# Optimization experiments

Hardware: AMD Instinct MI355X
Metric: run time of the kernel (lower is better)

Reference implementation:

```python
import jax, jax.numpy as jnp
import numpy as np

N_USERS, N_ITEMS, D = 16384, 8192, 64
IMG_D, TXT_D = 4096, 384
TOPK = 10
LAMBDA = 0.9         # args.lambda_coeff
NNZ = 786432
N_TOTAL = N_USERS + N_ITEMS


def l2norm(x, eps=1e-12):
    # F.normalize(p=2, dim=1)
    return x / jnp.maximum(jnp.linalg.norm(x, axis=-1, keepdims=True), eps)


def build_knn_graph(feats):
    """build_sim + build_knn_normalized_graph (sparse, sym norm).
    Returns row-sparse KNN graph as (values [N,k], indices [N,k])."""
    z = l2norm(feats)
    sim = z @ z.T                          # [N, N] cosine similarity
    vals, inds = jax.lax.top_k(sim, TOPK)  # [N, k]
    rowsum = vals.sum(axis=1)              # degree
    d_inv_sqrt = jnp.where(rowsum > 0, rowsum, 1.0) ** -0.5
    vals = vals * d_inv_sqrt[:, None] * d_inv_sqrt[inds]  # D^-1/2 A D^-1/2
    return vals, inds


def knn_mm(vals, inds, x):
    # sparse.mm with row-sparse [N,k] graph: out[i] = sum_k vals[i,k]*x[inds[i,k]]
    return jnp.einsum('nk,nkd->nd', vals, x[inds])


def setup_inputs() -> dict:
    key = jax.random.key(0)
    ks = jax.random.split(key, 16)
    xav = lambda k, shp: jax.random.normal(k, shp, jnp.float32) * (2.0 / (shp[0] + shp[-1])) ** 0.5
    return dict(
        adj_rows=jax.random.randint(ks[0], (NNZ,), 0, N_TOTAL, jnp.int32),
        adj_cols=jax.random.randint(ks[1], (NNZ,), 0, N_TOTAL, jnp.int32),
        adj_vals=jax.random.uniform(ks[2], (NNZ,), jnp.float32) / 32.0,
        image_feats=jax.random.normal(ks[3], (N_ITEMS, IMG_D), jnp.float32),
        text_feats=jax.random.normal(ks[4], (N_ITEMS, TXT_D), jnp.float32),
        user_emb=xav(ks[5], (N_USERS, D)),
        item_emb=xav(ks[6], (N_ITEMS, D)),
        img_w=xav(ks[7], (IMG_D, D)), img_b=jnp.zeros((D,), jnp.float32),
        txt_w=xav(ks[8], (TXT_D, D)), txt_b=jnp.zeros((D,), jnp.float32),
        q_w1=xav(ks[9], (D, D)), q_b1=jnp.zeros((D,), jnp.float32),
        q_w2=xav(ks[10], (D, 1)),
        gc_w=xav(ks[11], (2, D, D)), gc_b=jnp.zeros((2, D), jnp.float32),
        bi_w=xav(ks[12], (2, D, D)), bi_b=jnp.zeros((2, D), jnp.float32),
    )


def reference(adj_rows, adj_cols, adj_vals, image_feats, text_feats,
              user_emb, item_emb, img_w, img_b, txt_w, txt_b,
              q_w1, q_b1, q_w2, gc_w, gc_b, bi_w, bi_b):
    # original (init-time) modal graphs from raw features
    io_v, io_i = build_knn_graph(image_feats)
    to_v, to_i = build_knn_graph(text_feats)
    # projected modal features + dynamic graphs (build_item_graph=True)
    img_f = image_feats @ img_w + img_b
    txt_f = text_feats @ txt_w + txt_b
    in_v, in_i = build_knn_graph(img_f)
    tn_v, tn_i = build_knn_graph(txt_f)
    # one propagation layer over (1-l)*new_adj + l*orig_adj (separable for layers=1)
    e = item_emb
    img_e = (1 - LAMBDA) * knn_mm(in_v, in_i, e) + LAMBDA * knn_mm(io_v, io_i, e)
    txt_e = (1 - LAMBDA) * knn_mm(tn_v, tn_i, e) + LAMBDA * knn_mm(to_v, to_i, e)
    # attention-weighted fusion
    query = lambda x: jnp.tanh(x @ q_w1 + q_b1) @ q_w2   # [N_ITEMS, 1]
    att = jnp.concatenate([query(img_e), query(txt_e)], axis=-1)
    w = jax.nn.softmax(att, axis=-1)
    h = w[:, :1] * img_e + w[:, 1:] * txt_e
    # NGCF user-item propagation (dropout p=0 -> identity)
    ego = jnp.concatenate([user_emb, item_emb], axis=0)   # [N_TOTAL, D]
    all_e = [ego]
    for i in range(2):
        side = jax.ops.segment_sum(adj_vals[:, None] * ego[adj_cols], adj_rows,
                                   num_segments=N_TOTAL)
        s = jax.nn.leaky_relu(side @ gc_w[i] + gc_b[i])
        b = jax.nn.leaky_relu((ego * side) @ bi_w[i] + bi_b[i])
        ego = s + b
        all_e.append(l2norm(ego))
    all_e = jnp.mean(jnp.stack(all_e, axis=1), axis=1)
    u_g, i_g = all_e[:N_USERS], all_e[N_USERS:]
    i_g = i_g + l2norm(h)
    return u_g, i_g, img_e, txt_e, h
```

## Files before the change

### kernel.cpp

```cpp
#include <hip/hip_runtime.h>
#include <hip/hip_bf16.h>
#include <math.h>

#define N_USERS 16384
#define N_ITEMS 8192
#define N_TOTAL 24576
#define EMB_D 64
#define IMG_DIM 4096
#define TXT_DIM 384
#define K_TOP 10
#define N_CAND 16
#define NNZ_E 786432
#define NTILE 64
#define TRI_BLOCKS (NTILE * (NTILE + 1) / 2)
#define MIR_BLOCKS (NTILE * (NTILE - 1) / 2)
#define LDS_ST 129

typedef _Float16 f16x8 __attribute__((ext_vector_type(8)));
typedef float f32x4 __attribute__((ext_vector_type(4)));

#define AS1 __attribute__((address_space(1)))
#define AS3 __attribute__((address_space(3)))

__device__ __forceinline__ float leaky01(float x){ return x >= 0.f ? x : 0.01f * x; }

__device__ __forceinline__ void gld16(const void* g, void* l) {
  __builtin_amdgcn_global_load_lds((const AS1 unsigned int*)g, (AS3 unsigned int*)l, 16, 0, 0);
}

__device__ __forceinline__ bool beats(float v, int i, float u, int j) {
  return v > u || (v == u && i < j);
}

__device__ __forceinline__ float h2f(unsigned short u) {
  _Float16 h = __builtin_bit_cast(_Float16, u);
  return (float)h;
}
__device__ __forceinline__ unsigned short f2h(float v) {
  _Float16 h = (_Float16)v;
  return __builtin_bit_cast(unsigned short, h);
}

__global__ __launch_bounds__(256) void fill_map_k(int* __restrict__ map) {
  int b = blockIdx.x * 256 + threadIdx.x;
  if (b >= TRI_BLOCKS) return;
  int tileX, tileY;
  if (b < 1792) {
    int s = b >> 6, w = b & 63;
    int sy = 0, rem = 7;
    while (s >= rem) { s -= rem; sy++; rem--; }
    int sx = sy + 1 + s;
    tileY = sy * 8 + (w >> 3);
    tileX = sx * 8 + (w & 7);
  } else {
    int b2 = b - 1792;
    int sd = b2 / 36, w = b2 - sd * 36;
    int i = 0, rem = 8;
    while (w >= rem) { w -= rem; i++; rem--; }
    tileY = sd * 8 + i;
    tileX = sd * 8 + i + w;
  }
  map[b] = (tileY << 16) | tileX;
}

template<int TRI>
__global__ __launch_bounds__(256) void sim_mfma_k(const unsigned short* __restrict__ Zh,
                                                  unsigned short* __restrict__ C, int K, int r0,
                                                  const int* __restrict__ tile_map) {
  __shared__ unsigned short smA[128 * 32];
  __shared__ unsigned short smB[128 * 32];
  const int tid = threadIdx.x;
  const int lane = tid & 63;
  const int wid = tid >> 6;
  const int wr = wid >> 1, wc = wid & 1;

  int tileX, tileY;
  if (TRI) {
    int tm = tile_map[blockIdx.x];
    tileY = tm >> 16;
    tileX = tm & 0xffff;
  } else {
    tileX = blockIdx.x; tileY = blockIdx.y;
  }

  const int bRow = r0 + tileY * 128;
  const int bCol = tileX * 128;

  f32x4 acc[4][4];
  const f32x4 fzero = {0.f, 0.f, 0.f, 0.f};
  #pragma unroll
  for (int m = 0; m < 4; m++)
    #pragma unroll
    for (int n = 0; n < 4; n++) acc[m][n] = fzero;

  const int u0 = (wid * 2 + 0) * 64 + lane;
  const int u1 = (wid * 2 + 1) * 64 + lane;
  const int ar0 = u0 >> 2, ac0 = (u0 & 3) * 8;
  const int ar1 = u1 >> 2, ac1 = (u1 & 3) * 8;
  const unsigned offA0 = ((unsigned)(bRow + ar0) * (unsigned)K + (unsigned)ac0) * 2u;
  const unsigned offA1 = ((unsigned)(bRow + ar1) * (unsigned)K + (unsigned)ac1) * 2u;
  const unsigned offB0 = ((unsigned)(bCol + ar0) * (unsigned)K + (unsigned)ac0) * 2u;
  const unsigned offB1 = ((unsigned)(bCol + ar1) * (unsigned)K + (unsigned)ac1) * 2u;
  const char* Zb = (const char*)Zh;
  unsigned short* ldsA0 = smA + (wid * 2 + 0) * 512;
  unsigned short* ldsA1 = smA + (wid * 2 + 1) * 512;
  unsigned short* ldsB0 = smB + (wid * 2 + 0) * 512;
  unsigned short* ldsB1 = smB + (wid * 2 + 1) * 512;

  const int kc = lane >> 4;
  const int fr = lane & 15;

  for (unsigned kb = 0; kb < (unsigned)K * 2u; kb += 64u) {
    __syncthreads();
    gld16(Zb + (offA0 + kb), ldsA0);
    gld16(Zb + (offA1 + kb), ldsA1);
    gld16(Zb + (offB0 + kb), ldsB0);
    gld16(Zb + (offB1 + kb), ldsB1);
    __syncthreads();

    f16x8 a[4], b[4];
    #pragma unroll
    for (int m = 0; m < 4; m++)
      a[m] = *(const f16x8*)&smA[(wr * 64 + m * 16 + fr) * 32 + kc * 8];
    #pragma unroll
    for (int n = 0; n < 4; n++)
      b[n] = *(const f16x8*)&smB[(wc * 64 + n * 16 + fr) * 32 + kc * 8];
    #pragma unroll
    for (int m = 0; m < 4; m++)
      #pragma unroll
      for (int n = 0; n < 4; n++)
        acc[m][n] = __builtin_amdgcn_mfma_f32_16x16x32_f16(a[m], b[n], acc[m][n], 0, 0, 0);
  }

  const int crow = tileY * 128 + wr * 64 + (lane >> 4) * 4;
  const int ccol = bCol + wc * 64 + (lane & 15);
  #pragma unroll
  for (int m = 0; m < 4; m++)
    #pragma unroll
    for (int n = 0; n < 4; n++)
      #pragma unroll
      for (int r = 0; r < 4; r++)
        C[(size_t)(crow + m * 16 + r) * N_ITEMS + ccol + n * 16] = f2h(acc[m][n][r]);
}

__global__ __launch_bounds__(256) void tri_mirror_k(unsigned short* __restrict__ C) {
  __shared__ unsigned short t[128 * LDS_ST];
  int b = blockIdx.x;
  int ty = 0, rem = NTILE - 1;
  while (b >= rem) { b -= rem; ty++; rem--; }
  int tx = ty + 1 + b;
  const int tid = threadIdx.x;

  #pragma unroll
  for (int it = 0; it < 8; it++) {
    int idx = it * 2048 + tid * 8;
    int r = idx >> 7, c = idx & 127;
    uint4 v = *(const uint4*)&C[(size_t)(ty * 128 + r) * N_ITEMS + tx * 128 + c];
    const unsigned short* pv = (const unsigned short*)&v;
    #pragma unroll
    for (int j = 0; j < 8; j++) t[r * LDS_ST + c + j] = pv[j];
  }
  __syncthreads();

  #pragma unroll
  for (int it = 0; it < 8; it++) {
    int idx = it * 2048 + tid * 8;
    int orow = idx >> 7;
    int ocol = idx & 127;
    unsigned short buf[8];
    #pragma unroll
    for (int j = 0; j < 8; j++) buf[j] = t[(ocol + j) * LDS_ST + orow];
    *(uint4*)&C[(size_t)(tx * 128 + orow) * N_ITEMS + ty * 128 + ocol] = *(const uint4*)buf;
  }
}

__device__ __forceinline__ void ins4(float val, int idx, float tv[4], int ti[4]) {
  if (beats(val, idx, tv[3], ti[3])) {
    tv[3] = val; ti[3] = idx;
    if (beats(tv[3], ti[3], tv[2], ti[2])) { float a=tv[2];int b=ti[2]; tv[2]=tv[3];ti[2]=ti[3]; tv[3]=a;ti[3]=b; }
    if (beats(tv[2], ti[2], tv[1], ti[1])) { float a=tv[1];int b=ti[1]; tv[1]=tv[2];ti[1]=ti[2]; tv[2]=a;ti[2]=b; }
    if (beats(tv[1], ti[1], tv[0], ti[0])) { float a=tv[0];int b=ti[0]; tv[0]=tv[1];ti[0]=ti[1]; tv[1]=a;ti[1]=b; }
  }
}

__global__ __launch_bounds__(256) void topk16h_k(const unsigned short* __restrict__ sim,
                                                 int r0, int* __restrict__ cand) {
  int row = blockIdx.x * 4 + (threadIdx.x >> 6);
  int lane = threadIdx.x & 63;
  const uint4* s8 = reinterpret_cast<const uint4*>(sim + (size_t)row * N_ITEMS);

  float tv[4]; int ti[4];
  #pragma unroll
  for (int k = 0; k < 4; k++) { tv[k] = -INFINITY; ti[k] = 0x7fffffff; }
  unsigned long long ext0 = 0ull, ext1 = 0ull;

  for (int i = 0; i < 16; i++) {
    uint4 v = s8[i * 64 + lane];
    int base = (i * 64 + lane) * 8;
    ins4(h2f(v.x & 0xffff), base + 0, tv, ti);
    ins4(h2f(v.x >> 16),    base + 1, tv, ti);
    ins4(h2f(v.y & 0xffff), base + 2, tv, ti);
    ins4(h2f(v.y >> 16),    base + 3, tv, ti);
    ins4(h2f(v.z & 0xffff), base + 4, tv, ti);
    ins4(h2f(v.z >> 16),    base + 5, tv, ti);
    ins4(h2f(v.w & 0xffff), base + 6, tv, ti);
    ins4(h2f(v.w >> 16),    base + 7, tv, ti);
  }
  int nvalid = 4;
  for (int t = 0; t < N_CAND; t++) {
    float bv = tv[0]; int bi = ti[0];
    for (int o = 32; o; o >>= 1) {
      float ov = __shfl_xor(bv, o, 64);
      int   oi = __shfl_xor(bi, o, 64);
      if (beats(ov, oi, bv, bi)) { bv = ov; bi = oi; }
    }
    if (tv[0] == bv && ti[0] == bi) {
      int slot = ((bi >> 9) << 3) | (bi & 7);
      if (slot < 64) ext0 |= 1ull << slot; else ext1 |= 1ull << (slot - 64);
      tv[0]=tv[1];ti[0]=ti[1]; tv[1]=tv[2];ti[1]=ti[2]; tv[2]=tv[3];ti[2]=ti[3];
      tv[3]=-INFINITY; ti[3]=0x7fffffff;
      nvalid--;
      if (nvalid == 0) {
        for (int i = 0; i < 16; i++) {
          uint4 v = s8[i * 64 + lane];
          int base = (i * 64 + lane) * 8;
          float vv[8] = {h2f(v.x & 0xffff), h2f(v.x >> 16), h2f(v.y & 0xffff), h2f(v.y >> 16),
                         h2f(v.z & 0xffff), h2f(v.z >> 16), h2f(v.w & 0xffff), h2f(v.w >> 16)};
          #pragma unroll
          for (int q = 0; q < 8; q++) {
            int slot2 = i * 8 + q;
            bool used = (slot2 < 64) ? ((ext0 >> slot2) & 1ull) : ((ext1 >> (slot2 - 64)) & 1ull);
            if (!used) ins4(vv[q], base + q, tv, ti);
          }
        }
        nvalid = 4;
      }
    }
    if (lane == 0) cand[(size_t)(r0 + row) * N_CAND + t] = bi;
  }
}

__global__ __launch_bounds__(256) void refine_k(const float* __restrict__ X, int K,
                                                const float* __restrict__ invn,
                                                const int* __restrict__ cand,
                                                float* __restrict__ vals, int* __restrict__ inds,
                                                float* __restrict__ dis) {
  __shared__ __align__(16) float xr[4096];
  __shared__ float dots[N_CAND];
  int row = blockIdx.x;
  int tid = threadIdx.x, lane = tid & 63, wid = tid >> 6;
  for (int j = tid; j < K; j += 256) xr[j] = X[(size_t)row * K + j];
  __syncthreads();
  for (int c = wid; c < N_CAND; c += 4) {
    int ci = cand[(size_t)row * N_CAND + c];
    const float* xc = X + (size_t)ci * K;
    float p = 0.f;
    if (K == 4096) {
      const float4* xc4 = reinterpret_cast<const float4*>(xc);
      const float4* xr4 = reinterpret_cast<const float4*>(xr);
      for (int it = 0; it < 16; it++) {
        float4 a = xr4[it * 64 + lane];
        float4 g = xc4[it * 64 + lane];
        p += a.x * g.x + a.y * g.y + a.z * g.z + a.w * g.w;
      }
    } else {
      for (int j = lane; j < K; j += 64) p += xr[j] * xc[j];
    }
    for (int o = 32; o; o >>= 1) p += __shfl_xor(p, o, 64);
    if (lane == 0) dots[c] = p;
  }
  __syncthreads();
  if (tid == 0) {
    float v[N_CAND]; int id[N_CAND];
    float ir = invn[row];
    for (int c = 0; c < N_CAND; c++) {
      id[c] = cand[(size_t)row * N_CAND + c];
      v[c] = dots[c] * ir * invn[id[c]];
    }
    for (int a = 1; a < N_CAND; a++) {
      float av = v[a]; int ai = id[a];
      int b = a - 1;
      while (b >= 0 && beats(av, ai, v[b], id[b])) { v[b+1]=v[b]; id[b+1]=id[b]; b--; }
      v[b+1] = av; id[b+1] = ai;
    }
    float sum = 0.f;
    for (int t = 0; t < K_TOP; t++) {
      vals[(size_t)row * K_TOP + t] = v[t];
      inds[(size_t)row * K_TOP + t] = id[t];
      sum += v[t];
    }
    float rs = sum > 0.f ? sum : 1.0f;
    dis[row] = 1.0f / sqrtf(rs);
  }
}

__global__ __launch_bounds__(256) void scale_vals_k(float* __restrict__ vals,
                                                    const int* __restrict__ inds,
                                                    const float* __restrict__ dis, int tot) {
  int idx = blockIdx.x * 256 + threadIdx.x;
  if (idx < tot) {
    int i = idx / K_TOP;
    vals[idx] *= dis[i] * dis[inds[idx]];
  }
}

__global__ __launch_bounds__(256) void norm_cast_fused_k(const float* __restrict__ x,
                                                         float* __restrict__ invn,
                                                         unsigned short* __restrict__ zh, int K) {
  __shared__ __align__(16) float xr[4096];
  __shared__ float red[256];
  int r = blockIdx.x;
  const float* xp = x + (size_t)r * K;
  float ss = 0.f;
  for (int j = threadIdx.x; j < K; j += 256) { float v = xp[j]; xr[j] = v; ss += v * v; }
  red[threadIdx.x] = ss; __syncthreads();
  for (int s = 128; s > 0; s >>= 1) {
    if (threadIdx.x < s) red[threadIdx.x] += red[threadIdx.x + s];
    __syncthreads();
  }
  float inv = 1.f / fmaxf(sqrtf(red[0]), 1e-12f);
  if (threadIdx.x == 0) invn[r] = inv;
  for (int j = threadIdx.x; j < K; j += 256) {
    zh[(size_t)r * K + j] = f2h(xr[j] * inv);
  }
}

__global__ __launch_bounds__(256) void linear_splitk_k(const float* __restrict__ X,
                                                       const float* __restrict__ W,
                                                       const float* __restrict__ b,
                                                       float* __restrict__ outp, int K, int KS) {
  __shared__ float As[64][17];
  __shared__ float Ws[16][64];
  int br = blockIdx.x, ks = blockIdx.y;
  int tid = threadIdx.x, tr = tid >> 4, tc = tid & 15;
  int k0 = ks * KS, k1 = k0 + KS;
  int lrow = tid >> 2, lk = (tid & 3) * 4;
  int wrow = tid >> 4, wcol = (tid & 15) * 4;
  float acc[4][4] = {};
  for (int kb = k0; kb < k1; kb += 16) {
    __syncthreads();
    float4 xv = *(const float4*)&X[(size_t)(br * 64 + lrow) * K + kb + lk];
    As[lrow][lk + 0] = xv.x; As[lrow][lk + 1] = xv.y;
    As[lrow][lk + 2] = xv.z; As[lrow][lk + 3] = xv.w;
    *(float4*)&Ws[wrow][wcol] = *(const float4*)&W[(size_t)(kb + wrow) * 64 + wcol];
    __syncthreads();
    #pragma unroll
    for (int k = 0; k < 16; k++) {
      float a[4], w[4];
      #pragma unroll
      for (int i = 0; i < 4; i++) a[i] = As[tr * 4 + i][k];
      #pragma unroll
      for (int j = 0; j < 4; j++) w[j] = Ws[k][tc * 4 + j];
      #pragma unroll
      for (int i = 0; i < 4; i++)
        #pragma unroll
        for (int j = 0; j < 4; j++) acc[i][j] += a[i] * w[j];
    }
  }
  #pragma unroll
  for (int i = 0; i < 4; i++)
    #pragma unroll
    for (int j = 0; j < 4; j++) {
      float v = acc[i][j];
      if (ks == 0) v += b[tc * 4 + j];
      atomicAdd(&outp[(size_t)(br * 64 + tr * 4 + i) * 64 + tc * 4 + j], v);
    }
}

__global__ __launch_bounds__(256) void fuse_knn_k(const float* __restrict__ av, const int* __restrict__ ai,
                                                  const float* __restrict__ bv, const int* __restrict__ bi_,
                                                  const float* __restrict__ e, float* __restrict__ outp,
                                                  float lam) {
  int i = blockIdx.x * 4 + (threadIdx.x >> 6), d = threadIdx.x & 63;
  float sa = 0.f, sb = 0.f;
  #pragma unroll
  for (int k = 0; k < K_TOP; k++) {
    sa += av[(size_t)i * K_TOP + k] * e[(size_t)ai[(size_t)i * K_TOP + k] * 64 + d];
    sb += bv[(size_t)i * K_TOP + k] * e[(size_t)bi_[(size_t)i * K_TOP + k] * 64 + d];
  }
  outp[(size_t)i * 64 + d] = (1.f - lam) * sa + lam * sb;
}

__global__ __launch_bounds__(64) void attn_k(const float* __restrict__ img_e, const float* __restrict__ txt_e,
                                             const float* __restrict__ qw1, const float* __restrict__ qb1,
                                             const float* __restrict__ qw2, float* __restrict__ h) {
  __shared__ float W1[64][64];
  __shared__ float sI[64], sT[64];
  int t = threadIdx.x; int i = blockIdx.x;
  for (int k = 0; k < 64; k++) W1[k][t] = qw1[k * 64 + t];
  sI[t] = img_e[(size_t)i * 64 + t];
  sT[t] = txt_e[(size_t)i * 64 + t];
  __syncthreads();
  float yi = qb1[t], yt = qb1[t];
  #pragma unroll 16
  for (int k = 0; k < 64; k++) { yi += sI[k] * W1[k][t]; yt += sT[k] * W1[k][t]; }
  float w2 = qw2[t];
  float pi = tanhf(yi) * w2, pt = tanhf(yt) * w2;
  for (int o = 32; o > 0; o >>= 1) { pi += __shfl_xor(pi, o, 64); pt += __shfl_xor(pt, o, 64); }
  float m = fmaxf(pi, pt);
  float ei = expf(pi - m), et = expf(pt - m);
  float den = ei + et;
  float w0 = ei / den, w1v = et / den;
  h[(size_t)i * 64 + t] = w0 * sI[t] + w1v * sT[t];
}

__global__ __launch_bounds__(256) void hist_k(const int* __restrict__ rows, int* __restrict__ cnt) {
  int e = blockIdx.x * 256 + threadIdx.x;
  if (e < NNZ_E) atomicAdd(&cnt[rows[e]], 1);
}

__global__ __launch_bounds__(256) void scan_k(const int* __restrict__ cnt,
                                              int* __restrict__ starts,
                                              int* __restrict__ cursor) {
  __shared__ int part[256];
  int t = threadIdx.x;
  int base = t * (N_TOTAL / 256);
  int s = 0;
  for (int j = 0; j < N_TOTAL / 256; j++) s += cnt[base + j];
  part[t] = s;
  __syncthreads();
  for (int off = 1; off < 256; off <<= 1) {
    int v = part[t];
    int u = (t >= off) ? part[t - off] : 0;
    __syncthreads();
    part[t] = v + u;
    __syncthreads();
  }
  int run = (t > 0) ? part[t - 1] : 0;
  for (int j = 0; j < N_TOTAL / 256; j++) {
    starts[base + j] = run;
    cursor[base + j] = run;
    run += cnt[base + j];
  }
  if (t == 255) starts[N_TOTAL] = run;
}

__global__ __launch_bounds__(256) void place_k(const int* __restrict__ rows,
                                               const int* __restrict__ cols,
                                               const float* __restrict__ vals,
                                               int* __restrict__ cursor,
                                               int* __restrict__ cols_s,
                                               float* __restrict__ vals_s) {
  int e = blockIdx.x * 256 + threadIdx.x;
  if (e < NNZ_E) {
    int p = atomicAdd(&cursor[rows[e]], 1);
    cols_s[p] = cols[e];
    vals_s[p] = vals[e];
  }
}

__global__ __launch_bounds__(256) void gather_gcn_k(const int* __restrict__ starts,
                                                    const int* __restrict__ cols_s,
                                                    const float* __restrict__ vals_s,
                                                    const float* __restrict__ ego,
                                                    float* __restrict__ side) {
  int row = blockIdx.x * 4 + (threadIdx.x >> 6);
  int d = threadIdx.x & 63;
  int s = starts[row], e = starts[row + 1];
  float acc = 0.f;
  for (int i = s; i < e; i++) {
    acc += vals_s[i] * ego[(size_t)cols_s[i] * 64 + d];
  }
  side[(size_t)row * 64 + d] = acc;
}

__global__ __launch_bounds__(256) void gcn_k(const float* __restrict__ side, const float* __restrict__ ego,
                                             const float* __restrict__ gw, const float* __restrict__ gb,
                                             const float* __restrict__ bw, const float* __restrict__ bb,
                                             float* __restrict__ outp) {
  __shared__ float W1[64][64], W2[64][64];
  __shared__ float S[4][64], E[4][64];
  int t = threadIdx.x & 63, rb = threadIdx.x >> 6;
  int r = blockIdx.x * 4 + rb;
  for (int idx = threadIdx.x; idx < 4096; idx += 256) {
    W1[idx >> 6][idx & 63] = gw[idx];
    W2[idx >> 6][idx & 63] = bw[idx];
  }
  S[rb][t] = side[(size_t)r * 64 + t];
  E[rb][t] = ego[(size_t)r * 64 + t];
  __syncthreads();
  float s = gb[t], b = bb[t];
  #pragma unroll 16
  for (int k = 0; k < 64; k++) {
    float sv = S[rb][k];
    s += sv * W1[k][t];
    b += E[rb][k] * sv * W2[k][t];
  }
  outp[(size_t)r * 64 + t] = leaky01(s) + leaky01(b);
}

__global__ __launch_bounds__(256) void l2acc_k(const float* __restrict__ ego, float* __restrict__ acc) {
  int r = blockIdx.x * 4 + (threadIdx.x >> 6), d = threadIdx.x & 63;
  float v = ego[(size_t)r * 64 + d];
  float ss = v * v;
  for (int o = 32; o > 0; o >>= 1) ss += __shfl_xor(ss, o, 64);
  float inv = 1.f / fmaxf(sqrtf(ss), 1e-12f);
  acc[(size_t)r * 64 + d] += v * inv;
}

__global__ __launch_bounds__(256) void init_ego_k(const float* __restrict__ ue, const float* __restrict__ ie,
                                                  float* __restrict__ ego, float* __restrict__ acc) {
  int r = blockIdx.x * 4 + (threadIdx.x >> 6), d = threadIdx.x & 63;
  float v = (r < N_USERS) ? ue[(size_t)r * 64 + d] : ie[(size_t)(r - N_USERS) * 64 + d];
  ego[(size_t)r * 64 + d] = v;
  acc[(size_t)r * 64 + d] = v;
}

__global__ __launch_bounds__(256) void final_k(const float* __restrict__ acc, const float* __restrict__ h,
                                               float* __restrict__ u_g, float* __restrict__ i_g) {
  int r = blockIdx.x * 4 + (threadIdx.x >> 6), d = threadIdx.x & 63;
  float m = acc[(size_t)r * 64 + d] * (1.0f / 3.0f);
  if (r < N_USERS) {
    u_g[(size_t)r * 64 + d] = m;
  } else {
    int i = r - N_USERS;
    float hv = h[(size_t)i * 64 + d];
    float ss = hv * hv;
    for (int o = 32; o > 0; o >>= 1) ss += __shfl_xor(ss, o, 64);
    float inv = 1.f / fmaxf(sqrtf(ss), 1e-12f);
    i_g[(size_t)i * 64 + d] = m + hv * inv;
  }
}

static void build_graph(hipStream_t stream, const float* feats, int K, float* invn,
                        unsigned short* zh, unsigned short* sim, int stripe, int* cand,
                        const int* tile_map, float* vals, int* inds, float* dis) {
  norm_cast_fused_k<<<N_ITEMS, 256, 0, stream>>>(feats, invn, zh, K);
  if (stripe >= N_ITEMS) {
    sim_mfma_k<1><<<TRI_BLOCKS, 256, 0, stream>>>(zh, sim, K, 0, tile_map);
    tri_mirror_k<<<MIR_BLOCKS, 256, 0, stream>>>(sim);
    topk16h_k<<<N_ITEMS / 4, 256, 0, stream>>>(sim, 0, cand);
  } else {
    for (int r0 = 0; r0 < N_ITEMS; r0 += stripe) {
      int rows = (N_ITEMS - r0) < stripe ? (N_ITEMS - r0) : stripe;
      dim3 g(N_ITEMS / 128, rows / 128);
      sim_mfma_k<0><<<g, 256, 0, stream>>>(zh, sim, K, r0, tile_map);
      topk16h_k<<<rows / 4, 256, 0, stream>>>(sim, r0, cand);
    }
  }
  refine_k<<<N_ITEMS, 256, 0, stream>>>(feats, K, invn, cand, vals, inds, dis);
  int tot = N_ITEMS * K_TOP;
  scale_vals_k<<<(tot + 255) / 256, 256, 0, stream>>>(vals, inds, dis, tot);
}

extern "C" void kernel_launch(void* const* d_in, const int* in_sizes, int n_in,
                              void* d_out, int out_size, void* d_ws, size_t ws_size,
                              hipStream_t stream) {
  const int*   adj_rows   = (const int*)d_in[0];
  const int*   adj_cols   = (const int*)d_in[1];
  const float* adj_vals   = (const float*)d_in[2];
  const float* image_feats= (const float*)d_in[3];
  const float* text_feats = (const float*)d_in[4];
  const float* user_emb   = (const float*)d_in[5];
  const float* item_emb   = (const float*)d_in[6];
  const float* img_w      = (const float*)d_in[7];
  const float* img_b      = (const float*)d_in[8];
  const float* txt_w      = (const float*)d_in[9];
  const float* txt_b      = (const float*)d_in[10];
  const float* q_w1       = (const float*)d_in[11];
  const float* q_b1       = (const float*)d_in[12];
  const float* q_w2       = (const float*)d_in[13];
  const float* gc_w       = (const float*)d_in[14];
  const float* gc_b       = (const float*)d_in[15];
  const float* bi_w       = (const float*)d_in[16];
  const float* bi_b       = (const float*)d_in[17];

  float* out  = (float*)d_out;
  float* u_g  = out;
  float* i_g  = u_g + (size_t)N_USERS * 64;
  float* imgE = i_g + (size_t)N_ITEMS * 64;
  float* txtE = imgE + (size_t)N_ITEMS * 64;
  float* hOut = txtE + (size_t)N_ITEMS * 64;

  float* W = (float*)d_ws;
  size_t off = 0;
  auto alloc = [&](size_t n) { float* q = W + off; off += n; return q; };
  float* inv_io = alloc(N_ITEMS);
  float* inv_to = alloc(N_ITEMS);
  float* inv_in = alloc(N_ITEMS);
  float* inv_tn = alloc(N_ITEMS);
  float* img_f  = alloc((size_t)N_ITEMS * 64);
  float* txt_f  = alloc((size_t)N_ITEMS * 64);
  float* vals0 = alloc(N_ITEMS * K_TOP); int* inds0 = (int*)alloc(N_ITEMS * K_TOP);
  float* vals1 = alloc(N_ITEMS * K_TOP); int* inds1 = (int*)alloc(N_ITEMS * K_TOP);
  float* vals2 = alloc(N_ITEMS * K_TOP); int* inds2 = (int*)alloc(N_ITEMS * K_TOP);
  float* vals3 = alloc(N_ITEMS * K_TOP); int* inds3 = (int*)alloc(N_ITEMS * K_TOP);
  float* dis0 = alloc(N_ITEMS);
  float* dis1 = alloc(N_ITEMS);
  float* dis2 = alloc(N_ITEMS);
  float* dis3 = alloc(N_ITEMS);
  int*   cand = (int*)alloc((size_t)N_ITEMS * N_CAND);
  int*   tile_map = (int*)alloc(TRI_BLOCKS);
  float* ego_a = alloc((size_t)N_TOTAL * 64);
  float* ego_b = alloc((size_t)N_TOTAL * 64);
  float* side  = alloc((size_t)N_TOTAL * 64);
  float* acc   = alloc((size_t)N_TOTAL * 64);
  int* csr_cnt    = (int*)alloc(N_TOTAL);
  int* csr_starts = (int*)alloc(N_TOTAL + 1);
  int* csr_cursor = (int*)alloc(N_TOTAL);
  int* csr_cols   = (int*)alloc(NNZ_E);
  float* csr_vals = alloc(NNZ_E);
  unsigned short* zh = (unsigned short*)alloc(((size_t)N_ITEMS * IMG_DIM) / 2);
  unsigned short* sim = (unsigned short*)(W + off);

  size_t used_bytes = off * 4;
  size_t avail_b = (ws_size > used_bytes) ? (ws_size - used_bytes) : 0;
  long stripe_l = (long)((avail_b / ((size_t)N_ITEMS * 2)) / 128) * 128;
  if (stripe_l > N_ITEMS) stripe_l = N_ITEMS;
  if (stripe_l < 128) stripe_l = 128;
  int stripe = (int)stripe_l;

  fill_map_k<<<(TRI_BLOCKS + 255) / 256, 256, 0, stream>>>(tile_map);

  hipMemsetAsync(csr_cnt, 0, N_TOTAL * sizeof(int), stream);
  hist_k<<<(NNZ_E + 255) / 256, 256, 0, stream>>>(adj_rows, csr_cnt);
  scan_k<<<1, 256, 0, stream>>>(csr_cnt, csr_starts, csr_cursor);
  place_k<<<(NNZ_E + 255) / 256, 256, 0, stream>>>(adj_rows, adj_cols, adj_vals,
                                                   csr_cursor, csr_cols, csr_vals);

  build_graph(stream, image_feats, IMG_DIM, inv_io, zh, sim, stripe, cand, tile_map, vals0, inds0, dis0);
  build_graph(stream, text_feats,  TXT_DIM, inv_to, zh, sim, stripe, cand, tile_map, vals1, inds1, dis1);

  hipMemsetAsync(img_f, 0, (size_t)N_ITEMS * 64 * sizeof(float), stream);
  hipMemsetAsync(txt_f, 0, (size_t)N_ITEMS * 64 * sizeof(float), stream);
  linear_splitk_k<<<dim3(N_ITEMS / 64, 4), 256, 0, stream>>>(image_feats, img_w, img_b, img_f, IMG_DIM, IMG_DIM / 4);
  linear_splitk_k<<<dim3(N_ITEMS / 64, 4), 256, 0, stream>>>(text_feats,  txt_w, txt_b, txt_f, TXT_DIM, TXT_DIM / 4);

  build_graph(stream, img_f, 64, inv_in, zh, sim, stripe, cand, tile_map, vals2, inds2, dis2);
  build_graph(stream, txt_f, 64, inv_tn, zh, sim, stripe, cand, tile_map, vals3, inds3, dis3);

  const float lam = 0.9f;
  fuse_knn_k<<<N_ITEMS / 4, 256, 0, stream>>>(vals2, inds2, vals0, inds0, item_emb, imgE, lam);
  fuse_knn_k<<<N_ITEMS / 4, 256, 0, stream>>>(vals3, inds3, vals1, inds1, item_emb, txtE, lam);

  attn_k<<<N_ITEMS, 64, 0, stream>>>(imgE, txtE, q_w1, q_b1, q_w2, hOut);

  init_ego_k<<<N_TOTAL / 4, 256, 0, stream>>>(user_emb, item_emb, ego_a, acc);

  gather_gcn_k<<<N_TOTAL / 4, 256, 0, stream>>>(csr_starts, csr_cols, csr_vals, ego_a, side);
  gcn_k<<<N_TOTAL / 4, 256, 0, stream>>>(side, ego_a, gc_w, gc_b, bi_w, bi_b, ego_b);
  l2acc_k<<<N_TOTAL / 4, 256, 0, stream>>>(ego_b, acc);

  gather_gcn_k<<<N_TOTAL / 4, 256, 0, stream>>>(csr_starts, csr_cols, csr_vals, ego_b, side);
  gcn_k<<<N_TOTAL / 4, 256, 0, stream>>>(side, ego_b, gc_w + 4096, gc_b + 64, bi_w + 4096, bi_b + 64, ego_a);
  l2acc_k<<<N_TOTAL / 4, 256, 0, stream>>>(ego_a, acc);

  final_k<<<N_TOTAL / 4, 256, 0, stream>>>(acc, hOut, u_g, i_g);
}
```

Measured before the change: 2.406 ms.

## Store triangular sim tiles as fp32, then convert and mirror in one pass

The triangular MFMA kernel now writes fp32 tiles to a separate fp32 buffer. A new conv_mirror kernel, covering all triangle tiles, converts them to fp16, writes the upper tile and the transposed mirror tile. The fp16 conversion thus moves out of the GEMM epilogue into the mirror pass. This doubles the bytes the GEMM writes and adds an extra full fp32 read, and it needs the workspace to hold both a half and a float similarity matrix, falling back to the striped path otherwise.

```diff
diff --git a/kernel.cpp b/kernel.cpp
--- a/kernel.cpp
+++ b/kernel.cpp
@@ -13,7 +13,6 @@
 #define NNZ_E 786432
 #define NTILE 64
 #define TRI_BLOCKS (NTILE * (NTILE + 1) / 2)
-#define MIR_BLOCKS (NTILE * (NTILE - 1) / 2)
 #define LDS_ST 129
 
 typedef _Float16 f16x8 __attribute__((ext_vector_type(8)));
@@ -63,10 +62,9 @@
   map[b] = (tileY << 16) | tileX;
 }
 
-template<int TRI>
-__global__ __launch_bounds__(256) void sim_mfma_k(const unsigned short* __restrict__ Zh,
-                                                  unsigned short* __restrict__ C, int K, int r0,
-                                                  const int* __restrict__ tile_map) {
+__global__ __launch_bounds__(256) void sim_mfma_tri_k(const unsigned short* __restrict__ Zh,
+                                                      float* __restrict__ C, int K,
+                                                      const int* __restrict__ tile_map) {
   __shared__ unsigned short smA[128 * 32];
   __shared__ unsigned short smB[128 * 32];
   const int tid = threadIdx.x;
@@ -74,16 +72,10 @@
   const int wid = tid >> 6;
   const int wr = wid >> 1, wc = wid & 1;
 
-  int tileX, tileY;
-  if (TRI) {
-    int tm = tile_map[blockIdx.x];
-    tileY = tm >> 16;
-    tileX = tm & 0xffff;
-  } else {
-    tileX = blockIdx.x; tileY = blockIdx.y;
-  }
-
-  const int bRow = r0 + tileY * 128;
+  int tm = tile_map[blockIdx.x];
+  const int tileY = tm >> 16;
+  const int tileX = tm & 0xffff;
+  const int bRow = tileY * 128;
   const int bCol = tileX * 128;
 
   f32x4 acc[4][4];
@@ -132,6 +124,75 @@
         acc[m][n] = __builtin_amdgcn_mfma_f32_16x16x32_f16(a[m], b[n], acc[m][n], 0, 0, 0);
   }
 
+  const int crow = bRow + wr * 64 + (lane >> 4) * 4;
+  const int ccol = bCol + wc * 64 + (lane & 15);
+  #pragma unroll
+  for (int m = 0; m < 4; m++)
+    #pragma unroll
+    for (int n = 0; n < 4; n++)
+      #pragma unroll
+      for (int r = 0; r < 4; r++)
+        C[(size_t)(crow + m * 16 + r) * N_ITEMS + ccol + n * 16] = acc[m][n][r];
+}
+
+__global__ __launch_bounds__(256) void sim_mfma_rect_k(const unsigned short* __restrict__ Zh,
+                                                       unsigned short* __restrict__ C, int K, int r0) {
+  __shared__ unsigned short smA[128 * 32];
+  __shared__ unsigned short smB[128 * 32];
+  const int tid = threadIdx.x;
+  const int lane = tid & 63;
+  const int wid = tid >> 6;
+  const int wr = wid >> 1, wc = wid & 1;
+  const int tileX = blockIdx.x, tileY = blockIdx.y;
+
+  const int bRow = r0 + tileY * 128;
+  const int bCol = tileX * 128;
+
+  f32x4 acc[4][4];
+  const f32x4 fzero = {0.f, 0.f, 0.f, 0.f};
+  #pragma unroll
+  for (int m = 0; m < 4; m++)
+    #pragma unroll
+    for (int n = 0; n < 4; n++) acc[m][n] = fzero;
+
+  const int u0 = (wid * 2 + 0) * 64 + lane;
+  const int u1 = (wid * 2 + 1) * 64 + lane;
+  const int ar0 = u0 >> 2, ac0 = (u0 & 3) * 8;
+  const int ar1 = u1 >> 2, ac1 = (u1 & 3) * 8;
+  const size_t rowA0 = (size_t)(bRow + ar0) * K;
+  const size_t rowA1 = (size_t)(bRow + ar1) * K;
+  const size_t rowB0 = (size_t)(bCol + ar0) * K;
+  const size_t rowB1 = (size_t)(bCol + ar1) * K;
+  unsigned short* ldsA0 = smA + (wid * 2 + 0) * 512;
+  unsigned short* ldsA1 = smA + (wid * 2 + 1) * 512;
+  unsigned short* ldsB0 = smB + (wid * 2 + 0) * 512;
+  unsigned short* ldsB1 = smB + (wid * 2 + 1) * 512;
+
+  const int kc = lane >> 4;
+  const int fr = lane & 15;
+
+  for (int k0 = 0; k0 < K; k0 += 32) {
+    __syncthreads();
+    gld16(Zh + rowA0 + k0 + ac0, ldsA0);
+    gld16(Zh + rowA1 + k0 + ac1, ldsA1);
+    gld16(Zh + rowB0 + k0 + ac0, ldsB0);
+    gld16(Zh + rowB1 + k0 + ac1, ldsB1);
+    __syncthreads();
+
+    f16x8 a[4], b[4];
+    #pragma unroll
+    for (int m = 0; m < 4; m++)
+      a[m] = *(const f16x8*)&smA[(wr * 64 + m * 16 + fr) * 32 + kc * 8];
+    #pragma unroll
+    for (int n = 0; n < 4; n++)
+      b[n] = *(const f16x8*)&smB[(wc * 64 + n * 16 + fr) * 32 + kc * 8];
+    #pragma unroll
+    for (int m = 0; m < 4; m++)
+      #pragma unroll
+      for (int n = 0; n < 4; n++)
+        acc[m][n] = __builtin_amdgcn_mfma_f32_16x16x32_f16(a[m], b[n], acc[m][n], 0, 0, 0);
+  }
+
   const int crow = tileY * 128 + wr * 64 + (lane >> 4) * 4;
   const int ccol = bCol + wc * 64 + (lane & 15);
   #pragma unroll
@@ -143,23 +204,30 @@
         C[(size_t)(crow + m * 16 + r) * N_ITEMS + ccol + n * 16] = f2h(acc[m][n][r]);
 }
 
-__global__ __launch_bounds__(256) void tri_mirror_k(unsigned short* __restrict__ C) {
+__global__ __launch_bounds__(256) void conv_mirror_k(const float* __restrict__ Cf,
+                                                     unsigned short* __restrict__ Ch,
+                                                     const int* __restrict__ tile_map) {
   __shared__ unsigned short t[128 * LDS_ST];
-  int b = blockIdx.x;
-  int ty = 0, rem = NTILE - 1;
-  while (b >= rem) { b -= rem; ty++; rem--; }
-  int tx = ty + 1 + b;
+  int tm = tile_map[blockIdx.x];
+  const int ty = tm >> 16;
+  const int tx = tm & 0xffff;
   const int tid = threadIdx.x;
 
   #pragma unroll
   for (int it = 0; it < 8; it++) {
     int idx = it * 2048 + tid * 8;
     int r = idx >> 7, c = idx & 127;
-    uint4 v = *(const uint4*)&C[(size_t)(ty * 128 + r) * N_ITEMS + tx * 128 + c];
-    const unsigned short* pv = (const unsigned short*)&v;
-    #pragma unroll
-    for (int j = 0; j < 8; j++) t[r * LDS_ST + c + j] = pv[j];
-  }
+    const float* src = &Cf[(size_t)(ty * 128 + r) * N_ITEMS + tx * 128 + c];
+    float4 v0 = *(const float4*)(src);
+    float4 v1 = *(const float4*)(src + 4);
+    unsigned short buf[8];
+    buf[0] = f2h(v0.x); buf[1] = f2h(v0.y); buf[2] = f2h(v0.z); buf[3] = f2h(v0.w);
+    buf[4] = f2h(v1.x); buf[5] = f2h(v1.y); buf[6] = f2h(v1.z); buf[7] = f2h(v1.w);
+    *(uint4*)&Ch[(size_t)(ty * 128 + r) * N_ITEMS + tx * 128 + c] = *(const uint4*)buf;
+    #pragma unroll
+    for (int j = 0; j < 8; j++) t[r * LDS_ST + c + j] = buf[j];
+  }
+  if (tx == ty) return;
   __syncthreads();
 
   #pragma unroll
@@ -170,7 +238,7 @@
     unsigned short buf[8];
     #pragma unroll
     for (int j = 0; j < 8; j++) buf[j] = t[(ocol + j) * LDS_ST + orow];
-    *(uint4*)&C[(size_t)(tx * 128 + orow) * N_ITEMS + ty * 128 + ocol] = *(const uint4*)buf;
+    *(uint4*)&Ch[(size_t)(tx * 128 + orow) * N_ITEMS + ty * 128 + ocol] = *(const uint4*)buf;
   }
 }
 
@@ -523,19 +591,20 @@
 }
 
 static void build_graph(hipStream_t stream, const float* feats, int K, float* invn,
-                        unsigned short* zh, unsigned short* sim, int stripe, int* cand,
-                        const int* tile_map, float* vals, int* inds, float* dis) {
+                        unsigned short* zh, unsigned short* simh, float* simf,
+                        int tri_ok, int stripe, int* cand, const int* tile_map,
+                        float* vals, int* inds, float* dis) {
   norm_cast_fused_k<<<N_ITEMS, 256, 0, stream>>>(feats, invn, zh, K);
-  if (stripe >= N_ITEMS) {
-    sim_mfma_k<1><<<TRI_BLOCKS, 256, 0, stream>>>(zh, sim, K, 0, tile_map);
-    tri_mirror_k<<<MIR_BLOCKS, 256, 0, stream>>>(sim);
-    topk16h_k<<<N_ITEMS / 4, 256, 0, stream>>>(sim, 0, cand);
+  if (tri_ok) {
+    sim_mfma_tri_k<<<TRI_BLOCKS, 256, 0, stream>>>(zh, simf, K, tile_map);
+    conv_mirror_k<<<TRI_BLOCKS, 256, 0, stream>>>(simf, simh, tile_map);
+    topk16h_k<<<N_ITEMS / 4, 256, 0, stream>>>(simh, 0, cand);
   } else {
     for (int r0 = 0; r0 < N_ITEMS; r0 += stripe) {
       int rows = (N_ITEMS - r0) < stripe ? (N_ITEMS - r0) : stripe;
       dim3 g(N_ITEMS / 128, rows / 128);
-      sim_mfma_k<0><<<g, 256, 0, stream>>>(zh, sim, K, r0, tile_map);
-      topk16h_k<<<rows / 4, 256, 0, stream>>>(sim, r0, cand);
+      sim_mfma_rect_k<<<g, 256, 0, stream>>>(zh, simh, K, r0);
+      topk16h_k<<<rows / 4, 256, 0, stream>>>(simh, r0, cand);
     }
   }
   refine_k<<<N_ITEMS, 256, 0, stream>>>(feats, K, invn, cand, vals, inds, dis);
@@ -601,14 +670,22 @@
   int* csr_cols   = (int*)alloc(NNZ_E);
   float* csr_vals = alloc(NNZ_E);
   unsigned short* zh = (unsigned short*)alloc(((size_t)N_ITEMS * IMG_DIM) / 2);
-  unsigned short* sim = (unsigned short*)(W + off);
-
+
+  const size_t simh_b = (size_t)N_ITEMS * N_ITEMS * 2;
+  const size_t simf_b = (size_t)N_ITEMS * N_ITEMS * 4;
   size_t used_bytes = off * 4;
   size_t avail_b = (ws_size > used_bytes) ? (ws_size - used_bytes) : 0;
-  long stripe_l = (long)((avail_b / ((size_t)N_ITEMS * 2)) / 128) * 128;
-  if (stripe_l > N_ITEMS) stripe_l = N_ITEMS;
-  if (stripe_l < 128) stripe_l = 128;
-  int stripe = (int)stripe_l;
+  unsigned short* simh = (unsigned short*)(W + off);
+  float* simf = (float*)((char*)simh + simh_b);
+  int tri_ok = (avail_b >= simh_b + simf_b);
+
+  int stripe = N_ITEMS;
+  if (!tri_ok) {
+    long stripe_l = (long)((avail_b / ((size_t)N_ITEMS * 2)) / 128) * 128;
+    if (stripe_l > N_ITEMS) stripe_l = N_ITEMS;
+    if (stripe_l < 128) stripe_l = 128;
+    stripe = (int)stripe_l;
+  }
 
   fill_map_k<<<(TRI_BLOCKS + 255) / 256, 256, 0, stream>>>(tile_map);
 
@@ -618,16 +695,16 @@
   place_k<<<(NNZ_E + 255) / 256, 256, 0, stream>>>(adj_rows, adj_cols, adj_vals,
                                                    csr_cursor, csr_cols, csr_vals);
 
-  build_graph(stream, image_feats, IMG_DIM, inv_io, zh, sim, stripe, cand, tile_map, vals0, inds0, dis0);
-  build_graph(stream, text_feats,  TXT_DIM, inv_to, zh, sim, stripe, cand, tile_map, vals1, inds1, dis1);
+  build_graph(stream, image_feats, IMG_DIM, inv_io, zh, simh, simf, tri_ok, stripe, cand, tile_map, vals0, inds0, dis0);
+  build_graph(stream, text_feats,  TXT_DIM, inv_to, zh, simh, simf, tri_ok, stripe, cand, tile_map, vals1, inds1, dis1);
 
   hipMemsetAsync(img_f, 0, (size_t)N_ITEMS * 64 * sizeof(float), stream);
   hipMemsetAsync(txt_f, 0, (size_t)N_ITEMS * 64 * sizeof(float), stream);
   linear_splitk_k<<<dim3(N_ITEMS / 64, 4), 256, 0, stream>>>(image_feats, img_w, img_b, img_f, IMG_DIM, IMG_DIM / 4);
   linear_splitk_k<<<dim3(N_ITEMS / 64, 4), 256, 0, stream>>>(text_feats,  txt_w, txt_b, txt_f, TXT_DIM, TXT_DIM / 4);
 
-  build_graph(stream, img_f, 64, inv_in, zh, sim, stripe, cand, tile_map, vals2, inds2, dis2);
-  build_graph(stream, txt_f, 64, inv_tn, zh, sim, stripe, cand, tile_map, vals3, inds3, dis3);
+  build_graph(stream, img_f, 64, inv_in, zh, simh, simf, tri_ok, stripe, cand, tile_map, vals2, inds2, dis2);
+  build_graph(stream, txt_f, 64, inv_tn, zh, simh, simf, tri_ok, stripe, cand, tile_map, vals3, inds3, dis3);
 
   const float lam = 0.9f;
   fuse_knn_k<<<N_ITEMS / 4, 256, 0, stream>>>(vals2, inds2, vals0, inds0, item_emb, imgE, lam);
```

After: 2.609 ms. 1.08x slower.
